# Kernel optimization log

Hardware: AMD Instinct MI355X
Metric: run time of the kernel (lower is better)

## Reference

```python
import jax, jax.numpy as jnp
import numpy as np

B, T, D, H, F = 2, 2048, 1024, 16, 4096
DH = D // H  # 64
EPS = 1e-5


def setup_inputs() -> dict:
    key = jax.random.key(0)
    ks = jax.random.split(key, 12)
    s = 0.02
    return {
        "embedding": jax.random.normal(ks[0], (B, T, D), dtype=jnp.float32),
        "Wq": jax.random.normal(ks[1], (H, D, DH), dtype=jnp.float32) * s,
        "Wk": jax.random.normal(ks[2], (H, D, DH), dtype=jnp.float32) * s,
        "Wv": jax.random.normal(ks[3], (H, D, DH), dtype=jnp.float32) * s,
        "Wo": jax.random.normal(ks[4], (D, D), dtype=jnp.float32) * s,
        "bo": jnp.zeros((D,), dtype=jnp.float32),
        "W1": jax.random.normal(ks[5], (D, F), dtype=jnp.float32) * s,
        "b1": jnp.zeros((F,), dtype=jnp.float32),
        "W2": jax.random.normal(ks[6], (F, D), dtype=jnp.float32) * s,
        "b2": jnp.zeros((D,), dtype=jnp.float32),
        "g1": jnp.ones((D,), dtype=jnp.float32),
        "be1": jnp.zeros((D,), dtype=jnp.float32),
        "g2": jnp.ones((D,), dtype=jnp.float32),
        "be2": jnp.zeros((D,), dtype=jnp.float32),
    }


def _layernorm(x, g, b):
    mu = jnp.mean(x, axis=-1, keepdims=True)
    var = jnp.mean(jnp.square(x - mu), axis=-1, keepdims=True)
    return (x - mu) * jax.lax.rsqrt(var + EPS) * g + b


def reference(embedding, Wq, Wk, Wv, Wo, bo, W1, b1, W2, b2, g1, be1, g2, be2):
    x = embedding  # [B, T, D]
    # per-head projections (no bias), stacked: [B, H, T, DH]
    q = jnp.einsum("btd,hde->bhte", x, Wq)
    k = jnp.einsum("btd,hde->bhte", x, Wk)
    v = jnp.einsum("btd,hde->bhte", x, Wv)
    scores = jnp.einsum("bhte,bhse->bhts", q, k)  # [B, H, T, T]
    mask = jnp.tril(jnp.ones((T, T), dtype=bool))
    # Original masks to -inf first, then scales; -inf * scale = -inf, so this
    # equals softmax(scale * scores) on the causal support.
    scale = DH ** (-0.5)
    scores = jnp.where(mask, scores * scale, -jnp.inf)
    attn = jax.nn.softmax(scores, axis=-1)
    o = jnp.einsum("bhts,bhse->bthe", attn, v).reshape(B, T, D)  # head concat
    attn_out = o @ Wo + bo
    a = x + _layernorm(attn_out, g1, be1)  # residual uses original input
    f = jax.nn.relu(a @ W1 + b1) @ W2 + b2
    out = x + _layernorm(f, g2, be2)  # NOTE: residual from x, as in source
    return out
```

## Files before the change

kernel.cpp:

```cpp
#include <hip/hip_runtime.h>
#include <hip/hip_bf16.h>


#define Bq_ 2
#define T_ 2048
#define D_ 1024
#define H_ 16
#define DH_ 64
#define F_ 4096
#define N_ (Bq_ * T_)
#define EPS_ 1e-5f
#define KP 72

typedef __hip_bfloat16 bf16;
typedef unsigned short u16;
typedef __attribute__((ext_vector_type(8))) short bfrag;
typedef __attribute__((ext_vector_type(4))) float f32x4;

__device__ __forceinline__ u16 f2b(float f) {
    bf16 h = __float2bfloat16(f);
    return *(u16*)&h;
}
__device__ __forceinline__ float b2f_bits(u16 u) {
    return __uint_as_float(((unsigned)u) << 16);
}

__device__ __forceinline__ int swz(int row, int col) {
    return (col & ~31) | ((((col >> 3) ^ (row >> 1)) & 3) << 3) | (col & 7);
}

template <int N>
__device__ __forceinline__ void vmwait() {
    asm volatile("s_waitcnt vmcnt(%0)" :: "i"(N) : "memory");
}

#define GLDS16(g, l) __builtin_amdgcn_global_load_lds( \
    (const __attribute__((address_space(1))) unsigned int*)(g), \
    (__attribute__((address_space(3))) unsigned int*)(l), 16, 0, 0)

__device__ __forceinline__ void xcd_remap(int gx, int& bx, int& by) {
    const int bid = blockIdx.x + gx * blockIdx.y;
    const int t8 = bid >> 3;
    bx = t8 % gx;
    by = (bid & 7) + 8 * (t8 / gx);
}

__device__ __forceinline__ void tc_body(
    float (*Ts)[65], const float* s, int spitch,
    u16* dst, int dpitch, int drow0, int kcol0)
{
    const int t = threadIdx.x;
    #pragma unroll
    for (int i = 0; i < 4; i++) {
        const int idx = t + i * 256;
        const int kk = idx >> 4;
        const int mm = (idx & 15) * 4;
        float4 v = *(const float4*)(s + (size_t)kk * spitch + mm);
        Ts[mm][kk] = v.x; Ts[mm + 1][kk] = v.y;
        Ts[mm + 2][kk] = v.z; Ts[mm + 3][kk] = v.w;
    }
    __syncthreads();
    const int mm = t >> 2;
    const int kk0 = (t & 3) * 16;
    u16 o[16];
    #pragma unroll
    for (int j = 0; j < 16; j++) o[j] = f2b(Ts[mm][kk0 + j]);
    const int dr = drow0 + mm;
    u16* drow = dst + (size_t)dr * dpitch;
    const int c0 = kcol0 + kk0;
    *(uint4*)&drow[swz(dr, c0)]     = *(uint4*)&o[0];
    *(uint4*)&drow[swz(dr, c0 + 8)] = *(uint4*)&o[8];
}

__global__ __launch_bounds__(256) void tcvt(
    const float* __restrict__ src, int spitch, int srow0, int scol0,
    u16* __restrict__ dst, int dpitch, int drow0)
{
    __shared__ float Ts[64][65];
    const int mb = blockIdx.x, kb = blockIdx.y;
    const float* s = src + (size_t)(srow0 + kb * 64) * spitch + scol0 + mb * 64;
    tc_body(Ts, s, spitch, dst, dpitch, drow0 + mb * 64, kb * 64);
}

__global__ __launch_bounds__(256) void tcvt_kv(
    const float* __restrict__ Wk, const float* __restrict__ Wv,
    u16* __restrict__ dst)
{
    __shared__ float Ts[64][65];
    const int kb = blockIdx.y, z = blockIdx.z;
    const int sel = z >> 4, zz = z & 15;
    const float* src = sel ? Wv : Wk;
    const float* s = src + (size_t)zz * 1024 * 64 + (size_t)(kb * 64) * 64;
    tc_body(Ts, s, 64, dst, 1024, sel * 1024 + zz * 64, kb * 64);
}

__global__ __launch_bounds__(256) void tcvt_ffn(
    const float* __restrict__ W1, const float* __restrict__ W2, int c,
    u16* __restrict__ W1T, u16* __restrict__ W2T)
{
    __shared__ float Ts[64][65];
    const int mb = blockIdx.x, kb = blockIdx.y, z = blockIdx.z;
    const float* src = z ? W2 : W1;
    const int spitch = z ? 1024 : 4096;
    const int srow0  = z ? c * 1024 : 0;
    const int scol0  = z ? 0 : c * 1024;
    u16* dst = z ? W2T : W1T;
    const float* s = src + (size_t)(srow0 + kb * 64) * spitch + scol0 + mb * 64;
    tc_body(Ts, s, spitch, dst, 1024, mb * 64, kb * 64);
}

template <int AF32, int SPLIT, int RELU, int ACC, int NT, int CSWZ, int WAVE, int VT>
__global__ __launch_bounds__(256) void cgemm(
    const void* __restrict__ A, int lda,
    const u16* __restrict__ BT,
    u16* __restrict__ C0, u16* __restrict__ C1, int ldc,
    int Kdim,
    const float* __restrict__ bias, int bias_off)
{
    static_assert(NT == 2 || NT == 4, "NT");
    static_assert(!AF32 || NT == 4, "AF32 path assumes BN=128");
    static_assert(!(AF32 && WAVE), "WAVE requires glds-only staging");
    static_assert(!VT || SPLIT, "VT requires SPLIT");
    constexpr int BN = NT * 32;
    constexpr int NBUF = (NT == 2) ? 5 : 4;
    constexpr int DPT  = NBUF - 1;
    constexpr int LPT  = 4 + NT;
    constexpr int BELEM = 64 * 32;
    constexpr int AELEM = NT * 16 * 32;
    constexpr int PBUF  = BELEM + AELEM;
    constexpr int SELEM = WAVE ? 4 * NBUF * PBUF
                               : 2 * BN * 32 + 2 * 128 * 32;
    __shared__ alignas(16) u16 SMEM[SELEM];

    const int tid = threadIdx.x;
    const int lane = tid & 63;
    const int w = tid >> 6;
    const int lo16 = lane & 15;
    const int quad = lane >> 4;
    const int wi = w >> 1, wj = w & 1;

    int bx, by;
    xcd_remap(gridDim.x, bx, by);
    const int m0 = bx * 128;
    const int n0 = by * BN;

    f32x4 acc[NT][4] = {};

    const int c8 = (lane & 3) * 8;
    const int r4 = lane >> 2;
    const int fcol = ((quad ^ ((lo16 >> 1) & 3)) << 3);

    const int nsteps = Kdim >> 5;

    if constexpr (WAVE) {
        const u16* Ab = (const u16*)A;
        u16* wbase = &SMEM[w * NBUF * PBUF];
        auto wstage = [&](int slot, int k0) {
            u16* bb = wbase + slot * PBUF;
            #pragma unroll
            for (int c = 0; c < 4; c++)
                GLDS16(BT + (size_t)(m0 + wj * 64 + c * 16 + r4) * Kdim + k0 + c8,
                       bb + c * 512);
            u16* ab = bb + BELEM;
            #pragma unroll
            for (int c = 0; c < NT; c++)
                GLDS16(Ab + (size_t)(n0 + wi * (NT * 16) + c * 16 + r4) * lda + k0 + c8,
                       ab + c * 512);
        };
        #pragma unroll
        for (int i = 0; i < DPT; i++) wstage(i, i * 32);
        int t = 0, cb = 0;
        for (; t + DPT <= nsteps; ++t) {
            vmwait<(DPT - 1) * LPT>();
            __builtin_amdgcn_sched_barrier(0);
            const u16* bb = wbase + cb * PBUF;
            const u16* ab = bb + BELEM;
            bfrag af[NT], bfv[4];
            #pragma unroll
            for (int it = 0; it < NT; it++)
                af[it] = *(const bfrag*)(ab + (it * 16 + lo16) * 32 + fcol);
            #pragma unroll
            for (int jt = 0; jt < 4; jt++)
                bfv[jt] = *(const bfrag*)(bb + (jt * 16 + lo16) * 32 + fcol);
            if (t + DPT < nsteps)
                wstage(cb == 0 ? NBUF - 1 : cb - 1, (t + DPT) * 32);
            __builtin_amdgcn_s_setprio(1);
            #pragma unroll
            for (int it = 0; it < NT; it++)
                #pragma unroll
                for (int jt = 0; jt < 4; jt++)
                    acc[it][jt] = __builtin_amdgcn_mfma_f32_16x16x32_bf16(
                        af[it], bfv[jt], acc[it][jt], 0, 0, 0);
            __builtin_amdgcn_s_setprio(0);
            cb = (cb + 1 == NBUF) ? 0 : cb + 1;
        }
        vmwait<0>();
        __builtin_amdgcn_sched_barrier(0);
        for (; t < nsteps; ++t) {
            const u16* bb = wbase + cb * PBUF;
            const u16* ab = bb + BELEM;
            bfrag af[NT], bfv[4];
            #pragma unroll
            for (int it = 0; it < NT; it++)
                af[it] = *(const bfrag*)(ab + (it * 16 + lo16) * 32 + fcol);
            #pragma unroll
            for (int jt = 0; jt < 4; jt++)
                bfv[jt] = *(const bfrag*)(bb + (jt * 16 + lo16) * 32 + fcol);
            #pragma unroll
            for (int it = 0; it < NT; it++)
                #pragma unroll
                for (int jt = 0; jt < 4; jt++)
                    acc[it][jt] = __builtin_amdgcn_mfma_f32_16x16x32_bf16(
                        af[it], bfv[jt], acc[it][jt], 0, 0, 0);
            cb = (cb + 1 == NBUF) ? 0 : cb + 1;
        }
    } else {
        u16* As_ = SMEM;
        u16* Bs_ = SMEM + 2 * BN * 32;
        const int br0 = w * 32 + r4;
        const int br1 = br0 + 16;
        auto stage = [&](int buf, int k0) {
            GLDS16(BT + (size_t)(m0 + br0) * Kdim + k0 + c8,
                   Bs_ + buf * 128 * 32 + (w * 2 + 0) * 512);
            GLDS16(BT + (size_t)(m0 + br1) * Kdim + k0 + c8,
                   Bs_ + buf * 128 * 32 + (w * 2 + 1) * 512);
            const int ar = tid >> 1;
            const int kh = (tid & 1) * 16;
            const float* ap = (const float*)A + (size_t)(n0 + ar) * lda + k0 + kh;
            float4 v0 = ((const float4*)ap)[0];
            float4 v1 = ((const float4*)ap)[1];
            float4 v2 = ((const float4*)ap)[2];
            float4 v3 = ((const float4*)ap)[3];
            uint4 a0, a1;
            a0.x = (unsigned)f2b(v0.x) | ((unsigned)f2b(v0.y) << 16);
            a0.y = (unsigned)f2b(v0.z) | ((unsigned)f2b(v0.w) << 16);
            a0.z = (unsigned)f2b(v1.x) | ((unsigned)f2b(v1.y) << 16);
            a0.w = (unsigned)f2b(v1.z) | ((unsigned)f2b(v1.w) << 16);
            a1.x = (unsigned)f2b(v2.x) | ((unsigned)f2b(v2.y) << 16);
            a1.y = (unsigned)f2b(v2.z) | ((unsigned)f2b(v2.w) << 16);
            a1.z = (unsigned)f2b(v3.x) | ((unsigned)f2b(v3.y) << 16);
            a1.w = (unsigned)f2b(v3.z) | ((unsigned)f2b(v3.w) << 16);
            u16* arow = As_ + buf * BN * 32 + ar * 32;
            *(uint4*)&arow[swz(ar, kh)] = a0;
            *(uint4*)&arow[swz(ar, kh + 8)] = a1;
        };
        stage(0, 0);
        __syncthreads();
        int cur = 0;
        for (int t = 0; t < nsteps; ++t) {
            if (t + 1 < nsteps) stage(cur ^ 1, (t + 1) * 32);
            bfrag af[NT], bfv[4];
            #pragma unroll
            for (int it = 0; it < NT; it++)
                af[it] = *(const bfrag*)(As_ + cur * BN * 32
                         + (wi * (NT * 16) + it * 16 + lo16) * 32 + fcol);
            #pragma unroll
            for (int jt = 0; jt < 4; jt++)
                bfv[jt] = *(const bfrag*)(Bs_ + cur * 128 * 32
                          + (wj * 64 + jt * 16 + lo16) * 32 + fcol);
            __builtin_amdgcn_s_setprio(1);
            #pragma unroll
            for (int it = 0; it < NT; it++)
                #pragma unroll
                for (int jt = 0; jt < 4; jt++)
                    acc[it][jt] = __builtin_amdgcn_mfma_f32_16x16x32_bf16(
                        af[it], bfv[jt], acc[it][jt], 0, 0, 0);
            __builtin_amdgcn_s_setprio(0);
            if (t + 1 < nsteps) {
                __syncthreads();
                cur ^= 1;
            }
        }
    }
    #pragma unroll
    for (int jt = 0; jt < 4; jt++) {
        const int col = m0 + wj * 64 + jt * 16 + lo16;
        const bool vhalf = SPLIT && (col >> 10);
        const int cc = SPLIT ? (col & 1023) : col;
        if (VT && vhalf) {
            #pragma unroll
            for (int it = 0; it < NT; it++) {
                const int rowb = n0 + wi * (NT * 16) + it * 16 + quad * 4;
                u16 pk[4];
                #pragma unroll
                for (int r = 0; r < 4; r++) pk[r] = f2b(acc[it][jt][r]);
                *(uint2*)(C1 + ((size_t)((rowb >> 11) * 1024 + cc)) * 2048
                          + (rowb & 2047)) = *(uint2*)pk;
            }
        } else {
            u16* Cp = vhalf ? C1 : C0;
            const float bv = bias ? bias[bias_off + col] : 0.f;
            #pragma unroll
            for (int it = 0; it < NT; it++) {
                #pragma unroll
                for (int r = 0; r < 4; r++) {
                    const int row = n0 + wi * (NT * 16) + it * 16 + quad * 4 + r;
                    float v = acc[it][jt][r] + bv;
                    if constexpr (RELU) v = fmaxf(v, 0.f);
                    const int ccs = CSWZ ? swz(row, cc) : cc;
                    u16* cp = Cp + (size_t)row * ldc + ccs;
                    if constexpr (ACC) v += b2f_bits(*cp);
                    *cp = f2b(v);
                }
            }
        }
    }
}

template <int AF32, int QKV, int RELU, int ACC>
__global__ __launch_bounds__(256) void mgemm(
    const void* __restrict__ A,
    const float* __restrict__ B0f, const float* __restrict__ B1f, const float* __restrict__ B2f,
    u16* __restrict__ C0, u16* __restrict__ C1, u16* __restrict__ C2,
    int ldb, int brow_off, int bcol_off,
    const float* __restrict__ bias, int bias_off)
{
    __shared__ alignas(16) u16 As[128][32];
    __shared__ alignas(16) u16 Bt[128][40];
    __shared__ alignas(16) float Bs32[32][132];

    const int tid = threadIdx.x;
    const int lane = tid & 63;
    const int w = tid >> 6;
    const int lo16 = lane & 15;
    const int quad = lane >> 4;
    const int wi = w >> 1, wj = w & 1;

    int bx, by;
    xcd_remap(gridDim.x, bx, by);
    const int m0 = bx * 128;
    const int n0 = by * 128;

    f32x4 acc[4][4] = {};

    const int ar  = tid >> 1;
    const int akh = (tid & 1) * 16;
    const int bmq = tid & 31;
    const int bkb = (tid >> 5) * 4;
    const int tm  = tid >> 1;
    const int tkh = (tid & 1) * 16;

    for (int k0 = 0; k0 < 1024; k0 += 32) {
        uint4 a0, a1;
        if constexpr (AF32) {
            const float* ap = (const float*)A + (size_t)(n0 + ar) * 1024 + k0 + akh;
            float4 v0 = ((const float4*)ap)[0];
            float4 v1 = ((const float4*)ap)[1];
            float4 v2 = ((const float4*)ap)[2];
            float4 v3 = ((const float4*)ap)[3];
            a0.x = (unsigned)f2b(v0.x) | ((unsigned)f2b(v0.y) << 16);
            a0.y = (unsigned)f2b(v0.z) | ((unsigned)f2b(v0.w) << 16);
            a0.z = (unsigned)f2b(v1.x) | ((unsigned)f2b(v1.y) << 16);
            a0.w = (unsigned)f2b(v1.z) | ((unsigned)f2b(v1.w) << 16);
            a1.x = (unsigned)f2b(v2.x) | ((unsigned)f2b(v2.y) << 16);
            a1.y = (unsigned)f2b(v2.z) | ((unsigned)f2b(v2.w) << 16);
            a1.z = (unsigned)f2b(v3.x) | ((unsigned)f2b(v3.y) << 16);
            a1.w = (unsigned)f2b(v3.z) | ((unsigned)f2b(v3.w) << 16);
        } else {
            const u16* ap = (const u16*)A + (size_t)(n0 + ar) * 1024 + k0 + akh;
            a0 = ((const uint4*)ap)[0];
            a1 = ((const uint4*)ap)[1];
        }
        #pragma unroll
        for (int kk = 0; kk < 4; kk++) {
            const int k = bkb + kk;
            const float* bp;
            if constexpr (QKV) {
                const int m = m0 + bmq * 4;
                const int sel = m >> 10;
                const int mm = m & 1023;
                const float* Wp = (sel == 0) ? B0f : ((sel == 1) ? B1f : B2f);
                bp = Wp + ((size_t)(mm >> 6) * 1024 + k0 + k) * 64 + (mm & 63);
            } else {
                bp = B0f + (size_t)(brow_off + k0 + k) * ldb + bcol_off + m0 + bmq * 4;
            }
            *(float4*)&Bs32[k][bmq * 4] = *(const float4*)bp;
        }
        __syncthreads();
        *(uint4*)&As[ar][akh] = a0;
        *(uint4*)&As[ar][akh + 8] = a1;
        {
            u16 t[16];
            #pragma unroll
            for (int i = 0; i < 16; i++) t[i] = f2b(Bs32[tkh + i][tm]);
            *(uint4*)&Bt[tm][tkh] = *(uint4*)&t[0];
            *(uint4*)&Bt[tm][tkh + 8] = *(uint4*)&t[8];
        }
        __syncthreads();
        bfrag af[4], bfv[4];
        #pragma unroll
        for (int it = 0; it < 4; it++)
            af[it] = *(const bfrag*)&As[wi * 64 + it * 16 + lo16][quad * 8];
        #pragma unroll
        for (int jt = 0; jt < 4; jt++)
            bfv[jt] = *(const bfrag*)&Bt[wj * 64 + jt * 16 + lo16][quad * 8];
        #pragma unroll
        for (int it = 0; it < 4; it++)
            #pragma unroll
            for (int jt = 0; jt < 4; jt++)
                acc[it][jt] = __builtin_amdgcn_mfma_f32_16x16x32_bf16(
                    af[it], bfv[jt], acc[it][jt], 0, 0, 0);
        __syncthreads();
    }
    #pragma unroll
    for (int jt = 0; jt < 4; jt++) {
        const int col = m0 + wj * 64 + jt * 16 + lo16;
        u16* Cp;
        int cc;
        if constexpr (QKV) {
            const int sel = col >> 10;
            cc = col & 1023;
            Cp = (sel == 0) ? C0 : ((sel == 1) ? C1 : C2);
        } else {
            Cp = C0;
            cc = col;
        }
        const float bv = bias ? bias[bias_off + col] : 0.f;
        #pragma unroll
        for (int it = 0; it < 4; it++) {
            #pragma unroll
            for (int r = 0; r < 4; r++) {
                const int row = n0 + wi * 64 + it * 16 + quad * 4 + r;
                float v = acc[it][jt][r] + bv;
                if constexpr (RELU) v = fmaxf(v, 0.f);
                u16* cp = Cp + (size_t)row * 1024 + cc;
                if constexpr (ACC) v += b2f_bits(*cp);
                *cp = f2b(v);
            }
        }
    }
}

__global__ __launch_bounds__(256) void fattn_kernel(
    u16* __restrict__ Q, const u16* __restrict__ Kg, const u16* __restrict__ Vg)
{
    const int bi = blockIdx.x;
    const int qp = bi & 15;
    const int h  = (bi >> 4) & 15;
    const int b  = bi >> 8;
    const int tid = threadIdx.x;
    const int w = tid >> 6;
    const int lane = tid & 63;
    const int lo16 = lane & 15;
    const int quad = lane >> 4;

    __shared__ alignas(16) u16 Ks[64][KP];
    __shared__ alignas(16) u16 Vt[64][KP];
    __shared__ alignas(16) u16 Ps[4][16][KP];

    const int sr = tid >> 2;
    const int ec = (tid & 3) * 16;
    const size_t vrow = ((size_t)(b * 1024 + h * 64 + sr)) * 2048;

    #pragma unroll 1
    for (int pi = 0; pi < 2; pi++) {
        const int qt = pi ? (31 - qp) : qp;
        const int q0 = qt * 64;
        const size_t qrow = (size_t)(b * T_ + q0 + w * 16 + lo16) * 1024 + h * 64;
        bfrag qa0 = *(const bfrag*)(Q + qrow + quad * 8);
        bfrag qa1 = *(const bfrag*)(Q + qrow + 32 + quad * 8);

        f32x4 oacc[4] = {};
        float m_r[4], l_r[4];
        #pragma unroll
        for (int r = 0; r < 4; r++) { m_r[r] = -3e38f; l_r[r] = 0.f; }

        uint4 ka, kb, va, vb;
        {
            const size_t grow = (size_t)(b * T_ + sr) * 1024 + h * 64 + ec;
            ka = *(const uint4*)(Kg + grow);
            kb = *(const uint4*)(Kg + grow + 8);
            va = *(const uint4*)(Vg + vrow + ec);
            vb = *(const uint4*)(Vg + vrow + ec + 8);
        }

        for (int st = 0; st <= qt; st++) {
            *(uint4*)&Ks[sr][ec] = ka;
            *(uint4*)&Ks[sr][ec + 8] = kb;
            *(uint4*)&Vt[sr][ec] = va;
            *(uint4*)&Vt[sr][ec + 8] = vb;
            __syncthreads();
            if (st < qt) {
                const size_t grow = (size_t)(b * T_ + (st + 1) * 64 + sr) * 1024
                                  + h * 64 + ec;
                ka = *(const uint4*)(Kg + grow);
                kb = *(const uint4*)(Kg + grow + 8);
                va = *(const uint4*)(Vg + vrow + (st + 1) * 64 + ec);
                vb = *(const uint4*)(Vg + vrow + (st + 1) * 64 + ec + 8);
            }

            float sv[4][4];
            #pragma unroll
            for (int nt = 0; nt < 4; nt++) {
                bfrag kb0 = *(const bfrag*)&Ks[nt * 16 + lo16][quad * 8];
                bfrag kb1 = *(const bfrag*)&Ks[nt * 16 + lo16][32 + quad * 8];
                f32x4 cs = {0.f, 0.f, 0.f, 0.f};
                cs = __builtin_amdgcn_mfma_f32_16x16x32_bf16(qa0, kb0, cs, 0, 0, 0);
                cs = __builtin_amdgcn_mfma_f32_16x16x32_bf16(qa1, kb1, cs, 0, 0, 0);
                #pragma unroll
                for (int r = 0; r < 4; r++) sv[nt][r] = cs[r] * 0.125f;
            }
            if (st == qt) {
                #pragma unroll
                for (int nt = 0; nt < 4; nt++)
                    #pragma unroll
                    for (int r = 0; r < 4; r++)
                        if (nt * 16 + lo16 > w * 16 + quad * 4 + r) sv[nt][r] = -3e38f;
            }
            #pragma unroll
            for (int r = 0; r < 4; r++) {
                float m = fmaxf(fmaxf(sv[0][r], sv[1][r]), fmaxf(sv[2][r], sv[3][r]));
                #pragma unroll
                for (int off = 1; off < 16; off <<= 1)
                    m = fmaxf(m, __shfl_xor(m, off, 64));
                float mnew = fmaxf(m_r[r], m);
                float alpha = __expf(m_r[r] - mnew);
                m_r[r] = mnew;
                float s = 0.f;
                #pragma unroll
                for (int nt = 0; nt < 4; nt++) {
                    sv[nt][r] = __expf(sv[nt][r] - mnew);
                    s += sv[nt][r];
                }
                #pragma unroll
                for (int off = 1; off < 16; off <<= 1)
                    s += __shfl_xor(s, off, 64);
                l_r[r] = l_r[r] * alpha + s;
                #pragma unroll
                for (int et = 0; et < 4; et++) oacc[et][r] *= alpha;
            }
            #pragma unroll
            for (int nt = 0; nt < 4; nt++)
                #pragma unroll
                for (int r = 0; r < 4; r++)
                    Ps[w][quad * 4 + r][nt * 16 + lo16] = f2b(sv[nt][r]);
            bfrag pa0 = *(const bfrag*)&Ps[w][lo16][quad * 8];
            bfrag pa1 = *(const bfrag*)&Ps[w][lo16][32 + quad * 8];
            #pragma unroll
            for (int et = 0; et < 4; et++) {
                bfrag vb0 = *(const bfrag*)&Vt[et * 16 + lo16][quad * 8];
                bfrag vb1 = *(const bfrag*)&Vt[et * 16 + lo16][32 + quad * 8];
                oacc[et] = __builtin_amdgcn_mfma_f32_16x16x32_bf16(pa0, vb0, oacc[et], 0, 0, 0);
                oacc[et] = __builtin_amdgcn_mfma_f32_16x16x32_bf16(pa1, vb1, oacc[et], 0, 0, 0);
            }
            __syncthreads();
        }
        #pragma unroll
        for (int r = 0; r < 4; r++) {
            float rl = 1.f / l_r[r];
            const int row = q0 + w * 16 + quad * 4 + r;
            u16* orow = Q + (size_t)(b * T_ + row) * 1024;
            #pragma unroll
            for (int et = 0; et < 4; et++)
                orow[swz(row, h * 64 + et * 16 + lo16)] = f2b(oacc[et][r] * rl);
        }
    }
}

template <int WF32, int OSWZ>
__global__ __launch_bounds__(256) void ln_kernel(
    const u16* __restrict__ src, const float* __restrict__ resid,
    const float* __restrict__ g, const float* __restrict__ be,
    u16* __restrict__ dstb, float* __restrict__ dstf)
{
    const int r = blockIdx.x;
    const int tid = threadIdx.x;
    uint2 raw = ((const uint2*)(src + (size_t)r * D_))[tid];
    float y[4];
    y[0] = __uint_as_float(raw.x << 16);
    y[1] = __uint_as_float(raw.x & 0xffff0000u);
    y[2] = __uint_as_float(raw.y << 16);
    y[3] = __uint_as_float(raw.y & 0xffff0000u);
    float s = y[0] + y[1] + y[2] + y[3];
    float sq = y[0]*y[0] + y[1]*y[1] + y[2]*y[2] + y[3]*y[3];
    #pragma unroll
    for (int o = 32; o > 0; o >>= 1) {
        s += __shfl_down(s, o, 64);
        sq += __shfl_down(sq, o, 64);
    }
    __shared__ float rs[4], rq[4];
    if ((tid & 63) == 0) { rs[tid >> 6] = s; rq[tid >> 6] = sq; }
    __syncthreads();
    const float S = rs[0] + rs[1] + rs[2] + rs[3];
    const float Qm = rq[0] + rq[1] + rq[2] + rq[3];
    const float mu = S * (1.f / (float)D_);
    const float var = fmaxf(Qm * (1.f / (float)D_) - mu * mu, 0.f);
    const float rstd = rsqrtf(var + EPS_);
    const int c = tid * 4;
    #pragma unroll
    for (int i = 0; i < 4; i++) {
        y[i] = (y[i] - mu) * rstd * g[c + i] + be[c + i]
             + resid[(size_t)r * D_ + c + i];
    }
    if constexpr (WF32) {
        float4 o = {y[0], y[1], y[2], y[3]};
        ((float4*)(dstf + (size_t)r * D_))[tid] = o;
    } else {
        uint2 o;
        o.x = (unsigned)f2b(y[0]) | ((unsigned)f2b(y[1]) << 16);
        o.y = (unsigned)f2b(y[2]) | ((unsigned)f2b(y[3]) << 16);
        const int cs = OSWZ ? swz(r, c) : c;
        *(uint2*)(dstb + (size_t)r * D_ + cs) = o;
    }
}

extern "C" void kernel_launch(void* const* d_in, const int* in_sizes, int n_in,
                              void* d_out, int out_size, void* d_ws, size_t ws_size,
                              hipStream_t stream)
{
    const float* emb = (const float*)d_in[0];
    const float* Wq  = (const float*)d_in[1];
    const float* Wk  = (const float*)d_in[2];
    const float* Wv  = (const float*)d_in[3];
    const float* Wo  = (const float*)d_in[4];
    const float* bo  = (const float*)d_in[5];
    const float* W1  = (const float*)d_in[6];
    const float* b1  = (const float*)d_in[7];
    const float* W2  = (const float*)d_in[8];
    const float* b2  = (const float*)d_in[9];
    const float* g1  = (const float*)d_in[10];
    const float* be1 = (const float*)d_in[11];
    const float* g2  = (const float*)d_in[12];
    const float* be2 = (const float*)d_in[13];

    u16* WS = (u16*)d_ws;
    u16* DO = (u16*)d_out;

    const size_t M1 = 1024 * 1024;
    u16* WkvT = WS;
    u16* Q    = WS;
    u16* Kb   = DO;
    u16* Vb   = DO + 4 * M1;
    u16* O    = WS;
    u16* WoT  = DO;
    u16* P    = DO + 4 * M1;
    u16* Af   = DO;
    u16* Hc   = DO + 4 * M1;
    u16* W1T  = DO + 6 * M1;
    u16* W2T  = DO + 7 * M1;
    u16* F    = WS;
    float* outf = (float*)d_out;

    const dim3 blk(256);

    tcvt_kv<<<dim3(1, 16, 32), blk, 0, stream>>>(Wk, Wv, WkvT);
    cgemm<1, 1, 0, 0, 4, 0, 0, 1><<<dim3(16, 32), blk, 0, stream>>>(
        emb, 1024, WkvT, Kb, Vb, 1024, 1024, nullptr, 0);
    mgemm<1, 1, 0, 0><<<dim3(8, 32), blk, 0, stream>>>(
        emb, Wq, Wq, Wq, Q, nullptr, nullptr, 0, 0, 0, nullptr, 0);
    fattn_kernel<<<Bq_ * H_ * 16, blk, 0, stream>>>(Q, Kb, Vb);
    tcvt<<<dim3(16, 16), blk, 0, stream>>>(Wo, 1024, 0, 0, WoT, 1024, 0);
    cgemm<0, 0, 0, 0, 4, 0, 1, 0><<<dim3(8, 32), blk, 0, stream>>>(
        O, 1024, WoT, P, nullptr, 1024, 1024, bo, 0);
    ln_kernel<0, 1><<<N_, blk, 0, stream>>>(P, emb, g1, be1, Af, nullptr);
    for (int c = 0; c < 4; c++) {
        tcvt_ffn<<<dim3(16, 16, 2), blk, 0, stream>>>(W1, W2, c, W1T, W2T);
        for (int rh = 0; rh < 2; rh++) {
            u16* Afh = Af + (size_t)rh * 2048 * 1024;
            u16* Fh  = F  + (size_t)rh * 2048 * 1024;
            cgemm<0, 0, 1, 0, 2, 1, 1, 0><<<dim3(8, 32), blk, 0, stream>>>(
                Afh, 1024, W1T, Hc, nullptr, 1024, 1024, b1, c * 1024);
            if (c == 0) {
                cgemm<0, 0, 0, 0, 2, 0, 1, 0><<<dim3(8, 32), blk, 0, stream>>>(
                    Hc, 1024, W2T, Fh, nullptr, 1024, 1024, b2, 0);
            } else {
                cgemm<0, 0, 0, 1, 2, 0, 1, 0><<<dim3(8, 32), blk, 0, stream>>>(
                    Hc, 1024, W2T, Fh, nullptr, 1024, 1024, nullptr, 0);
            }
        }
    }
    ln_kernel<1, 0><<<N_, blk, 0, stream>>>(F, emb, g2, be2, nullptr, outf);
}
```

Measured before the change: 535.4 us.

## Double-buffer LDS fragment registers in wave-private GEMM loop

Restructures the wave-private GEMM main loop to ping-pong between two register fragment sets, loading the next step's A/B fragments from LDS while MFMAs on the current set run. The loop is unrolled by two, and the global-to-LDS staging and vmcnt waits are rescheduled with a remaining-step wait selector. This aims to hide LDS read latency behind matrix ops, at the cost of higher VGPR pressure and more complex wait logic. The loop also assumes nsteps is even.

```diff
diff --git a/kernel.cpp b/kernel.cpp
--- a/kernel.cpp
+++ b/kernel.cpp
@@ -167,52 +167,69 @@
                 GLDS16(Ab + (size_t)(n0 + wi * (NT * 16) + c * 16 + r4) * lda + k0 + c8,
                        ab + c * 512);
         };
-        #pragma unroll
-        for (int i = 0; i < DPT; i++) wstage(i, i * 32);
-        int t = 0, cb = 0;
-        for (; t + DPT <= nsteps; ++t) {
-            vmwait<(DPT - 1) * LPT>();
-            __builtin_amdgcn_sched_barrier(0);
-            const u16* bb = wbase + cb * PBUF;
+        auto rdfrags = [&](int slot, bfrag* af, bfrag* bv) {
+            const u16* bb = wbase + slot * PBUF;
             const u16* ab = bb + BELEM;
-            bfrag af[NT], bfv[4];
             #pragma unroll
             for (int it = 0; it < NT; it++)
                 af[it] = *(const bfrag*)(ab + (it * 16 + lo16) * 32 + fcol);
             #pragma unroll
             for (int jt = 0; jt < 4; jt++)
-                bfv[jt] = *(const bfrag*)(bb + (jt * 16 + lo16) * 32 + fcol);
-            if (t + DPT < nsteps)
-                wstage(cb == 0 ? NBUF - 1 : cb - 1, (t + DPT) * 32);
+                bv[jt] = *(const bfrag*)(bb + (jt * 16 + lo16) * 32 + fcol);
+        };
+        auto mma = [&](bfrag* af, bfrag* bv) {
             __builtin_amdgcn_s_setprio(1);
             #pragma unroll
             for (int it = 0; it < NT; it++)
                 #pragma unroll
                 for (int jt = 0; jt < 4; jt++)
                     acc[it][jt] = __builtin_amdgcn_mfma_f32_16x16x32_bf16(
-                        af[it], bfv[jt], acc[it][jt], 0, 0, 0);
+                        af[it], bv[jt], acc[it][jt], 0, 0, 0);
             __builtin_amdgcn_s_setprio(0);
-            cb = (cb + 1 == NBUF) ? 0 : cb + 1;
-        }
-        vmwait<0>();
+        };
+        auto waitsel = [&](int rem) {
+            if (rem >= DPT - 1)      vmwait<(DPT - 1) * LPT>();
+            else if (rem == 2)       vmwait<2 * LPT>();
+            else if (rem == 1)       vmwait<1 * LPT>();
+            else                     vmwait<0>();
+            __builtin_amdgcn_sched_barrier(0);
+        };
+
+        #pragma unroll
+        for (int i = 0; i < DPT; i++) wstage(i, i * 32);
+        vmwait<(DPT - 1) * LPT>();
         __builtin_amdgcn_sched_barrier(0);
-        for (; t < nsteps; ++t) {
-            const u16* bb = wbase + cb * PBUF;
-            const u16* ab = bb + BELEM;
-            bfrag af[NT], bfv[4];
-            #pragma unroll
-            for (int it = 0; it < NT; it++)
-                af[it] = *(const bfrag*)(ab + (it * 16 + lo16) * 32 + fcol);
-            #pragma unroll
-            for (int jt = 0; jt < 4; jt++)
-                bfv[jt] = *(const bfrag*)(bb + (jt * 16 + lo16) * 32 + fcol);
-            #pragma unroll
-            for (int it = 0; it < NT; it++)
-                #pragma unroll
-                for (int jt = 0; jt < 4; jt++)
-                    acc[it][jt] = __builtin_amdgcn_mfma_f32_16x16x32_bf16(
-                        af[it], bfv[jt], acc[it][jt], 0, 0, 0);
-            cb = (cb + 1 == NBUF) ? 0 : cb + 1;
+
+        bfrag afA[NT], bvA[4], afB[NT], bvB[4];
+        rdfrags(0, afA, bvA);
+
+        int ss = DPT;
+        int rs = 1;
+        for (int t = 0; t < nsteps; t += 2) {
+            if (t + DPT < nsteps) {
+                wstage(ss, (t + DPT) * 32);
+                ss = (ss + 1 == NBUF) ? 0 : ss + 1;
+            }
+            {
+                int rem = nsteps - 2 - t;
+                if (rem > DPT - 1) rem = DPT - 1;
+                waitsel(rem);
+                rdfrags(rs, afB, bvB);
+                rs = (rs + 1 == NBUF) ? 0 : rs + 1;
+            }
+            mma(afA, bvA);
+            if (t + 1 + DPT < nsteps) {
+                wstage(ss, (t + 1 + DPT) * 32);
+                ss = (ss + 1 == NBUF) ? 0 : ss + 1;
+            }
+            if (t + 2 < nsteps) {
+                int rem = nsteps - 3 - t;
+                if (rem > DPT - 1) rem = DPT - 1;
+                waitsel(rem);
+                rdfrags(rs, afA, bvA);
+                rs = (rs + 1 == NBUF) ? 0 : rs + 1;
+            }
+            mma(afB, bvB);
         }
     } else {
         u16* As_ = SMEM;
```

After: 559.6 us. 1.05x slower.
